# Optimization experiments

Hardware: AMD Instinct MI355X
Metric: run time of the kernel (lower is better)

The kernel has to match this reference:

```python
import jax, jax.numpy as jnp
import numpy as np

B, N, T, F_IN, H, E = 64, 325, 24, 64, 64, 2600
NEG_SLOPE = 0.2


def setup_inputs() -> dict:
    key = jax.random.key(0)
    k1, k2, k3, k4, k5 = jax.random.split(key, 5)
    x = jax.random.normal(k1, (B, N, T, F_IN), dtype=jnp.float32)
    edge_index = jax.random.randint(k2, (2, E), 0, N, dtype=jnp.int32)
    scale = 1.0 / np.sqrt(F_IN)
    W = jax.random.normal(k3, (H, F_IN), dtype=jnp.float32) * scale
    att_src = jax.random.normal(k4, (H,), dtype=jnp.float32) * scale
    att_dst = jax.random.normal(k5, (H,), dtype=jnp.float32) * scale
    bias = jnp.zeros((H,), dtype=jnp.float32)
    return {"x": x, "edge_index": edge_index, "W": W,
            "att_src": att_src, "att_dst": att_dst, "bias": bias}


def reference(x, edge_index, W, att_src, att_dst, bias):
    b, n, t, nf = x.shape
    # Fold the B*T graph replicas into one leading axis: [G, N, F]
    xg = x.transpose(0, 2, 1, 3).reshape(b * t, n, nf)
    h = jnp.einsum('gnf,hf->gnh', xg, W)  # linear transform [G, N, H]
    a_s = h @ att_src  # [G, N] per-node source attention logit
    a_d = h @ att_dst  # [G, N] per-node dest attention logit
    src, dst = edge_index[0], edge_index[1]
    # Per-edge raw score (gather), LeakyReLU as in GATConv: [G, E]
    e = jax.nn.leaky_relu(a_s[:, src] + a_d[:, dst], negative_slope=NEG_SLOPE)

    def per_graph(e_g, h_g):
        # segment softmax over edges grouped by destination node
        m = jax.ops.segment_max(e_g, dst, num_segments=n)
        ex = jnp.exp(e_g - m[dst])
        den = jax.ops.segment_sum(ex, dst, num_segments=n)
        alpha = ex / den[dst]  # [E]
        msg = alpha[:, None] * h_g[src]  # [E, H]
        return jax.ops.segment_sum(msg, dst, num_segments=n)  # [N, H]

    out = jax.vmap(per_graph)(e, h) + bias  # [G, N, H]
    out = jax.nn.gelu(out, approximate=False)
    # Faithful to source: view(B,T,N,H) then raw reshape(B,N,T,H) (row-major reinterpret)
    return out.reshape(b, n, t, -1)
```

## Files before the change

### kernel.cpp

```cpp
#include <hip/hip_runtime.h>
#include <hip/hip_bf16.h>

#define B_  64
#define N_  325
#define T_  24
#define F_  64
#define H_  64
#define E_  2600
#define G_  (B_ * T_)
#define BLK 512
#define GRID3 512
#define HS  68

using half2_t = __attribute__((ext_vector_type(2))) _Float16;
using half8_t = __attribute__((ext_vector_type(8))) _Float16;
using f32x4   = __attribute__((ext_vector_type(4))) float;

__global__ __launch_bounds__(512) void k_off_prep(
    const int* __restrict__ ei, const float* __restrict__ W,
    const float* __restrict__ att_src, const float* __restrict__ att_dst,
    int* __restrict__ csr_off, unsigned short* __restrict__ perm,
    float* __restrict__ w_sd) {
  __shared__ int cnt[N_];
  const int tid = threadIdx.x;
  for (int i = tid; i < N_; i += BLK) cnt[i] = 0;
  __syncthreads();
  for (int e = tid; e < E_; e += BLK) atomicAdd(&cnt[ei[E_ + e]], 1);
  __syncthreads();
  if (tid <= N_) {
    int off = 0;
    for (int m = 0; m < N_; ++m) off += (m < tid) ? cnt[m] : 0;
    csr_off[tid] = off;
  }
  if (tid < N_) {
    const int c = cnt[tid];
    int r = 0;
    for (int m = 0; m < N_; ++m) {
      const int cm = cnt[m];
      r += (cm > c || (cm == c && m < tid)) ? 1 : 0;
    }
    perm[r] = (unsigned short)tid;
  }
  if (tid < 128) {
    const int k = tid & 63;
    const float* av = (tid < 64) ? att_src : att_dst;
    float s = 0.f;
    for (int h = 0; h < H_; ++h) s += W[h * F_ + k] * av[h];
    w_sd[tid] = s;
  }
}

__global__ __launch_bounds__(64) void k_scatter(const int* __restrict__ ei,
                                                const int* __restrict__ csr_off,
                                                unsigned short* __restrict__ csr_src) {
  __shared__ int dsts[E_];
  const int tid = threadIdx.x;
  for (int i = tid; i < E_; i += 64) dsts[i] = ei[E_ + i];
  __syncthreads();
  const int e = blockIdx.x * 64 + tid;
  if (e >= E_) return;
  const int myd = dsts[e];
  int rank = 0;
#pragma unroll 4
  for (int k = 0; k < e; ++k) rank += (dsts[k] == myd) ? 1 : 0;
  csr_src[csr_off[myd] + rank] = (unsigned short)ei[e];
}

__device__ __forceinline__ float f16lo(unsigned u) {
  half2_t h = __builtin_bit_cast(half2_t, u); return (float)h[0];
}
__device__ __forceinline__ float f16hi(unsigned u) {
  half2_t h = __builtin_bit_cast(half2_t, u); return (float)h[1];
}
__device__ __forceinline__ unsigned short f16b(float f) {
  _Float16 h = (_Float16)f; return __builtin_bit_cast(unsigned short, h);
}
__device__ __forceinline__ half2_t pkrtz(float a, float b) {
  return __builtin_bit_cast(half2_t, __builtin_amdgcn_cvt_pkrtz(a, b));
}
__device__ __forceinline__ half8_t pk8(float4 a, float4 b) {
  half2_t p0 = pkrtz(a.x, a.y);
  half2_t p1 = pkrtz(a.z, a.w);
  half2_t p2 = pkrtz(b.x, b.y);
  half2_t p3 = pkrtz(b.z, b.w);
  half8_t r;
  r[0] = p0[0]; r[1] = p0[1]; r[2] = p1[0]; r[3] = p1[1];
  r[4] = p2[0]; r[5] = p2[1]; r[6] = p3[0]; r[7] = p3[1];
  return r;
}

__device__ __forceinline__ float gelu_f(float v) {
  float t = v * (1.5957691216f + 0.0713550903f * (v * v));
  t = fminf(t, 80.0f);
  float e = __expf(t);
  return v * e * __builtin_amdgcn_rcpf(e + 1.0f);
}

__global__ __launch_bounds__(512, 4) void k_gat5(
    const float* __restrict__ x, const int* __restrict__ csr_off_g,
    const unsigned short* __restrict__ csr_src_g,
    const unsigned short* __restrict__ perm_g, const float* __restrict__ W,
    const float* __restrict__ w_sd, const float* __restrict__ bias,
    float* __restrict__ out) {
  __shared__ _Float16 h_s[N_][HS];
  __shared__ unsigned short src_s[E_];
  __shared__ unsigned asad_s[N_];
  __shared__ unsigned short coff_s[N_ + 1];
  __shared__ unsigned short perm_s[N_];

  const int tid  = threadIdx.x;
  const int lane = tid & 63;
  const int wv   = tid >> 6;
  const int l15  = lane & 15;
  const int l4   = lane >> 4;

  for (int i = tid; i < E_; i += BLK) src_s[i] = csr_src_g[i];
  for (int i = tid; i <= N_; i += BLK) coff_s[i] = csr_off_g[i];
  for (int i = tid; i < N_; i += BLK) perm_s[i] = perm_g[i];

  half8_t bf[2][4];
#pragma unroll
  for (int ct = 0; ct < 4; ++ct)
#pragma unroll
    for (int k0 = 0; k0 < 2; ++k0) {
      const float* p = W + (size_t)(ct * 16 + l15) * F_ + k0 * 32 + l4 * 8;
      bf[k0][ct] = pk8(*(const float4*)p, *(const float4*)(p + 4));
    }

  half8_t bw[2];
  {
    const float* wp = w_sd + (l15 & 1) * 64;
#pragma unroll
    for (int k0 = 0; k0 < 2; ++k0) {
      half8_t z = {0, 0, 0, 0, 0, 0, 0, 0};
      const float* p = wp + k0 * 32 + l4 * 8;
      bw[k0] = (l15 < 2) ? pk8(*(const float4*)p, *(const float4*)(p + 4)) : z;
    }
  }

  const int l16v = tid & 15;
  const int qw   = tid >> 4;
  const float4 bias4 = *(const float4*)(bias + 4 * l16v);

  for (int gi = 0; gi < 3; ++gi) {
    const int g  = blockIdx.x + (gi << 9);
    const int bb = g / T_;
    const int tt = g % T_;
    if (gi) __syncthreads();

    const float* xg = x + ((size_t)bb * N_ * T_ + tt) * F_;
    float4 xa[3][4];
#pragma unroll
    for (int ti = 0; ti < 3; ++ti) {
      int t = wv + ti * 8; if (t > 20) t = 20;
      int rr = t * 16 + l15; if (rr > N_ - 1) rr = N_ - 1;
      const float* xr = xg + (size_t)rr * (T_ * F_) + l4 * 8;
      xa[ti][0] = *(const float4*)xr;
      xa[ti][1] = *(const float4*)(xr + 4);
      xa[ti][2] = *(const float4*)(xr + 32);
      xa[ti][3] = *(const float4*)(xr + 36);
    }
#pragma unroll
    for (int ti = 0; ti < 3; ++ti) {
      const int t = wv + ti * 8;
      if (t < 21) {
        const int r0 = t * 16;
        const half8_t a0 = pk8(xa[ti][0], xa[ti][1]);
        const half8_t a1 = pk8(xa[ti][2], xa[ti][3]);
        const bool full = (r0 + 16 <= N_);
#pragma unroll
        for (int ct = 0; ct < 4; ++ct) {
          f32x4 acc = {0.f, 0.f, 0.f, 0.f};
          acc = __builtin_amdgcn_mfma_f32_16x16x32_f16(a0, bf[0][ct], acc, 0, 0, 0);
          acc = __builtin_amdgcn_mfma_f32_16x16x32_f16(a1, bf[1][ct], acc, 0, 0, 0);
          const int col = ct * 16 + l15;
#pragma unroll
          for (int j = 0; j < 4; ++j) {
            const int row = r0 + l4 * 4 + j;
            if (full || row < N_) h_s[row][col] = (_Float16)acc[j];
          }
        }
        f32x4 acc2 = {0.f, 0.f, 0.f, 0.f};
        acc2 = __builtin_amdgcn_mfma_f32_16x16x32_f16(a0, bw[0], acc2, 0, 0, 0);
        acc2 = __builtin_amdgcn_mfma_f32_16x16x32_f16(a1, bw[1], acc2, 0, 0, 0);
        if (l15 < 2) {
#pragma unroll
          for (int j = 0; j < 4; ++j) {
            const int row = r0 + l4 * 4 + j;
            if (full || row < N_)
              ((unsigned short*)asad_s)[row * 2 + l15] = f16b(acc2[j]);
          }
        }
      }
    }
    __syncthreads();

    for (int idx = qw; idx < N_; idx += 32) {
      const int n   = perm_s[idx];
      const int beg = coff_s[n], end = coff_s[n + 1];
      const float adn = f16hi(asad_s[n]);
      half2_t a01 = {(_Float16)0.f, (_Float16)0.f};
      half2_t a23 = {(_Float16)0.f, (_Float16)0.f};
      float den = 0.f;
      for (int p = beg; p < end; ++p) {
        const int s = src_s[p];
        float e = f16lo(asad_s[s]) + adn;
        e = fmaxf(e, 0.2f * e);
        const float ex =
            __builtin_amdgcn_exp2f(__builtin_fmaf(e, 1.44269504f, -7.21347520f));
        den += ex;
        const half2_t al2 = pkrtz(ex, ex);
        const uint2 hv = *(const uint2*)&h_s[s][4 * l16v];
        a01 = al2 * __builtin_bit_cast(half2_t, hv.x) + a01;
        a23 = al2 * __builtin_bit_cast(half2_t, hv.y) + a23;
      }
      const float inv = (end > beg) ? __builtin_amdgcn_rcpf(den) : 0.0f;
      const float v0 = gelu_f((float)a01[0] * inv + bias4.x);
      const float v1 = gelu_f((float)a01[1] * inv + bias4.y);
      const float v2 = gelu_f((float)a23[0] * inv + bias4.z);
      const float v3 = gelu_f((float)a23[1] * inv + bias4.w);
      *(float4*)&out[((size_t)g * N_ + n) * H_ + 4 * l16v] =
          make_float4(v0, v1, v2, v3);
    }
  }
}

extern "C" void kernel_launch(void* const* d_in, const int* in_sizes, int n_in,
                              void* d_out, int out_size, void* d_ws, size_t ws_size,
                              hipStream_t stream) {
  (void)in_sizes; (void)n_in; (void)out_size; (void)ws_size;
  const float* x       = (const float*)d_in[0];
  const int*   ei      = (const int*)d_in[1];
  const float* W       = (const float*)d_in[2];
  const float* att_src = (const float*)d_in[3];
  const float* att_dst = (const float*)d_in[4];
  const float* bias    = (const float*)d_in[5];
  float* out = (float*)d_out;

  char* ws = (char*)d_ws;
  int*            csr_off = (int*)(ws + 0);
  unsigned short* csr_src = (unsigned short*)(ws + 4096);
  unsigned short* perm    = (unsigned short*)(ws + 16384);
  float*          w_sd    = (float*)(ws + 20480);

  k_off_prep<<<1, BLK, 0, stream>>>(ei, W, att_src, att_dst, csr_off, perm, w_sd);
  k_scatter<<<(E_ + 63) / 64, 64, 0, stream>>>(ei, csr_off, csr_src);
  k_gat5<<<GRID3, BLK, 0, stream>>>(x, csr_off, csr_src, perm, W, w_sd, bias, out);
}
```

Before: 127.4 us.

## Precompute per-edge softmax weights once and widen per-thread feature slice

Adds a per-edge pass that computes the exponentiated attention score once per edge and stores it alongside the source index in shared memory, rather than having all 16 lanes of a node's group recompute it. The aggregation loop now gives each thread 8 features (8 lanes per node) and uses 16-byte LDS loads, with the h row stride padded to 72 for alignment. It also stores destination indices in CSR order from the scatter kernel and moves the x loads inside the tile loop. The cost is an extra sync and an edge-pass per graph, plus larger shared memory for the edge array.

```diff
diff --git a/kernel.cpp b/kernel.cpp
--- a/kernel.cpp
+++ b/kernel.cpp
@@ -10,7 +10,7 @@
 #define G_  (B_ * T_)
 #define BLK 512
 #define GRID3 512
-#define HS  68
+#define HS  72
 
 using half2_t = __attribute__((ext_vector_type(2))) _Float16;
 using half8_t = __attribute__((ext_vector_type(8))) _Float16;
@@ -52,7 +52,8 @@
 
 __global__ __launch_bounds__(64) void k_scatter(const int* __restrict__ ei,
                                                 const int* __restrict__ csr_off,
-                                                unsigned short* __restrict__ csr_src) {
+                                                unsigned short* __restrict__ csr_src,
+                                                unsigned short* __restrict__ edst) {
   __shared__ int dsts[E_];
   const int tid = threadIdx.x;
   for (int i = tid; i < E_; i += 64) dsts[i] = ei[E_ + i];
@@ -63,7 +64,9 @@
   int rank = 0;
 #pragma unroll 4
   for (int k = 0; k < e; ++k) rank += (dsts[k] == myd) ? 1 : 0;
-  csr_src[csr_off[myd] + rank] = (unsigned short)ei[e];
+  const int pos = csr_off[myd] + rank;
+  csr_src[pos] = (unsigned short)ei[e];
+  edst[pos]    = (unsigned short)myd;
 }
 
 __device__ __forceinline__ float f16lo(unsigned u) {
@@ -96,14 +99,15 @@
   return v * e * __builtin_amdgcn_rcpf(e + 1.0f);
 }
 
-__global__ __launch_bounds__(512, 4) void k_gat5(
+__global__ __launch_bounds__(512, 4) void k_gat8(
     const float* __restrict__ x, const int* __restrict__ csr_off_g,
     const unsigned short* __restrict__ csr_src_g,
-    const unsigned short* __restrict__ perm_g, const float* __restrict__ W,
+    const unsigned short* __restrict__ perm_g,
+    const unsigned short* __restrict__ edst_g, const float* __restrict__ W,
     const float* __restrict__ w_sd, const float* __restrict__ bias,
     float* __restrict__ out) {
-  __shared__ _Float16 h_s[N_][HS];
-  __shared__ unsigned short src_s[E_];
+  __shared__ __align__(16) _Float16 h_s[N_][HS];
+  __shared__ uint2    edge_s[E_];
   __shared__ unsigned asad_s[N_];
   __shared__ unsigned short coff_s[N_ + 1];
   __shared__ unsigned short perm_s[N_];
@@ -114,7 +118,8 @@
   const int l15  = lane & 15;
   const int l4   = lane >> 4;
 
-  for (int i = tid; i < E_; i += BLK) src_s[i] = csr_src_g[i];
+  for (int i = tid; i < E_; i += BLK)
+    edge_s[i] = make_uint2(0u, (unsigned)csr_src_g[i]);
   for (int i = tid; i <= N_; i += BLK) coff_s[i] = csr_off_g[i];
   for (int i = tid; i < N_; i += BLK) perm_s[i] = perm_g[i];
 
@@ -138,9 +143,10 @@
     }
   }
 
-  const int l16v = tid & 15;
-  const int qw   = tid >> 4;
-  const float4 bias4 = *(const float4*)(bias + 4 * l16v);
+  const int l8 = tid & 7;
+  const int gq = tid >> 3;
+  const float4 biasA = *(const float4*)(bias + 8 * l8);
+  const float4 biasB = *(const float4*)(bias + 8 * l8 + 4);
 
   for (int gi = 0; gi < 3; ++gi) {
     const int g  = blockIdx.x + (gi << 9);
@@ -149,24 +155,20 @@
     if (gi) __syncthreads();
 
     const float* xg = x + ((size_t)bb * N_ * T_ + tt) * F_;
-    float4 xa[3][4];
-#pragma unroll
-    for (int ti = 0; ti < 3; ++ti) {
-      int t = wv + ti * 8; if (t > 20) t = 20;
-      int rr = t * 16 + l15; if (rr > N_ - 1) rr = N_ - 1;
-      const float* xr = xg + (size_t)rr * (T_ * F_) + l4 * 8;
-      xa[ti][0] = *(const float4*)xr;
-      xa[ti][1] = *(const float4*)(xr + 4);
-      xa[ti][2] = *(const float4*)(xr + 32);
-      xa[ti][3] = *(const float4*)(xr + 36);
-    }
 #pragma unroll
     for (int ti = 0; ti < 3; ++ti) {
       const int t = wv + ti * 8;
+      int tc = t > 20 ? 20 : t;
+      int rr = tc * 16 + l15; if (rr > N_ - 1) rr = N_ - 1;
+      const float* xr = xg + (size_t)rr * (T_ * F_) + l4 * 8;
+      const float4 u0 = *(const float4*)xr;
+      const float4 u1 = *(const float4*)(xr + 4);
+      const float4 u2 = *(const float4*)(xr + 32);
+      const float4 u3 = *(const float4*)(xr + 36);
       if (t < 21) {
         const int r0 = t * 16;
-        const half8_t a0 = pk8(xa[ti][0], xa[ti][1]);
-        const half8_t a1 = pk8(xa[ti][2], xa[ti][3]);
+        const half8_t a0 = pk8(u0, u1);
+        const half8_t a1 = pk8(u2, u3);
         const bool full = (r0 + 16 <= N_);
 #pragma unroll
         for (int ct = 0; ct < 4; ++ct) {
@@ -195,32 +197,48 @@
     }
     __syncthreads();
 
-    for (int idx = qw; idx < N_; idx += 32) {
+    for (int p = tid; p < E_; p += BLK) {
+      const unsigned sp = edge_s[p].y;
+      const int dp = edst_g[p];
+      float e = f16lo(asad_s[sp]) + f16hi(asad_s[dp]);
+      e = fmaxf(e, 0.2f * e);
+      const float ex =
+          __builtin_amdgcn_exp2f(__builtin_fmaf(e, 1.44269504f, -7.21347520f));
+      const unsigned ax = (unsigned)f16b(ex);
+      edge_s[p].x = ax | (ax << 16);
+    }
+    __syncthreads();
+
+    for (int idx = gq; idx < N_; idx += 64) {
       const int n   = perm_s[idx];
       const int beg = coff_s[n], end = coff_s[n + 1];
-      const float adn = f16hi(asad_s[n]);
       half2_t a01 = {(_Float16)0.f, (_Float16)0.f};
       half2_t a23 = {(_Float16)0.f, (_Float16)0.f};
+      half2_t a45 = {(_Float16)0.f, (_Float16)0.f};
+      half2_t a67 = {(_Float16)0.f, (_Float16)0.f};
       float den = 0.f;
       for (int p = beg; p < end; ++p) {
-        const int s = src_s[p];
-        float e = f16lo(asad_s[s]) + adn;
-        e = fmaxf(e, 0.2f * e);
-        const float ex =
-            __builtin_amdgcn_exp2f(__builtin_fmaf(e, 1.44269504f, -7.21347520f));
-        den += ex;
-        const half2_t al2 = pkrtz(ex, ex);
-        const uint2 hv = *(const uint2*)&h_s[s][4 * l16v];
-        a01 = al2 * __builtin_bit_cast(half2_t, hv.x) + a01;
-        a23 = al2 * __builtin_bit_cast(half2_t, hv.y) + a23;
+        const uint2 eu = edge_s[p];
+        den += f16lo(eu.x);
+        const half2_t al = __builtin_bit_cast(half2_t, eu.x);
+        const uint4 hv = *(const uint4*)&h_s[eu.y][8 * l8];
+        a01 = al * __builtin_bit_cast(half2_t, hv.x) + a01;
+        a23 = al * __builtin_bit_cast(half2_t, hv.y) + a23;
+        a45 = al * __builtin_bit_cast(half2_t, hv.z) + a45;
+        a67 = al * __builtin_bit_cast(half2_t, hv.w) + a67;
       }
       const float inv = (end > beg) ? __builtin_amdgcn_rcpf(den) : 0.0f;
-      const float v0 = gelu_f((float)a01[0] * inv + bias4.x);
-      const float v1 = gelu_f((float)a01[1] * inv + bias4.y);
-      const float v2 = gelu_f((float)a23[0] * inv + bias4.z);
-      const float v3 = gelu_f((float)a23[1] * inv + bias4.w);
-      *(float4*)&out[((size_t)g * N_ + n) * H_ + 4 * l16v] =
-          make_float4(v0, v1, v2, v3);
+      const float v0 = gelu_f((float)a01[0] * inv + biasA.x);
+      const float v1 = gelu_f((float)a01[1] * inv + biasA.y);
+      const float v2 = gelu_f((float)a23[0] * inv + biasA.z);
+      const float v3 = gelu_f((float)a23[1] * inv + biasA.w);
+      const float v4 = gelu_f((float)a45[0] * inv + biasB.x);
+      const float v5 = gelu_f((float)a45[1] * inv + biasB.y);
+      const float v6 = gelu_f((float)a67[0] * inv + biasB.z);
+      const float v7 = gelu_f((float)a67[1] * inv + biasB.w);
+      float* op = &out[((size_t)g * N_ + n) * H_ + 8 * l8];
+      *(float4*)op       = make_float4(v0, v1, v2, v3);
+      *(float4*)(op + 4) = make_float4(v4, v5, v6, v7);
     }
   }
 }
@@ -241,9 +259,11 @@
   int*            csr_off = (int*)(ws + 0);
   unsigned short* csr_src = (unsigned short*)(ws + 4096);
   unsigned short* perm    = (unsigned short*)(ws + 16384);
-  float*          w_sd    = (float*)(ws + 20480);
+  unsigned short* edst    = (unsigned short*)(ws + 20480);
+  float*          w_sd    = (float*)(ws + 28672);
 
   k_off_prep<<<1, BLK, 0, stream>>>(ei, W, att_src, att_dst, csr_off, perm, w_sd);
-  k_scatter<<<(E_ + 63) / 64, 64, 0, stream>>>(ei, csr_off, csr_src);
-  k_gat5<<<GRID3, BLK, 0, stream>>>(x, csr_off, csr_src, perm, W, w_sd, bias, out);
-}
+  k_scatter<<<(E_ + 63) / 64, 64, 0, stream>>>(ei, csr_off, csr_src, edst);
+  k_gat8<<<GRID3, BLK, 0, stream>>>(x, csr_off, csr_src, perm, edst, W, w_sd,
+                                    bias, out);
+}
```

New measurement: 116.0 us. 9.0% less time.
